# Performance work log

Measured on AMD Instinct MI355X. Metric: run time of the kernel, lower is better.

The kernel has to match this reference:

```python
import jax, jax.numpy as jnp
import numpy as np
from jax.scipy.special import logsumexp

NUM_JOINT_TYPES = 17
SINKHORN_ITERS = 30
SINKHORN_TAU = 0.05
BIG_COST = 1.0e6


def _scot_forward(embeddings, W1, b1, prototype_pool, joint_types, k):
    n = embeddings.shape[0]
    # node encoder: Linear + SELU
    h = jax.nn.selu(embeddings @ W1 + b1)  # [N, H]
    prototypes = prototype_pool[:k]        # [K, H] (k <= k_max)
    # squared euclidean distance (torch.cdist(p=2).pow(2))
    d2 = (jnp.sum(h * h, axis=1)[:, None]
          + jnp.sum(prototypes * prototypes, axis=1)[None, :]
          - 2.0 * (h @ prototypes.T))
    d2 = jnp.maximum(d2, 0.0)              # [N, K]
    # expand each person slot to 17 joint-type slots
    cost = jnp.repeat(d2, NUM_JOINT_TYPES, axis=1)          # [N, K*17]
    slot_types = jnp.tile(jnp.arange(NUM_JOINT_TYPES), k)   # [K*17]
    type_mask = joint_types[:, None] == slot_types[None, :]  # [N, K*17]
    cost = jnp.where(type_mask, cost, BIG_COST)

    n_slots = k * NUM_JOINT_TYPES
    log_K = -cost / SINKHORN_TAU
    log_K_ext = jnp.concatenate([log_K, jnp.zeros((n, 1), log_K.dtype)], axis=1)  # [N, K*17+1]
    # target marginal: 1 per slot, slack column absorbs leftover mass
    tm = jnp.ones(n_slots + 1, log_K.dtype).at[-1].set(float(max(n - n_slots, 1)))
    log_tm = jnp.log(tm)

    def step(carry, _):
        log_u, log_v = carry
        log_u = -logsumexp(log_K_ext + log_v[None, :], axis=1)   # row normalization
        log_v = log_tm - logsumexp(log_K_ext + log_u[:, None], axis=0)  # col normalization
        return (log_u, log_v), None

    init = (jnp.zeros(n, log_K.dtype), jnp.zeros(n_slots + 1, log_K.dtype))
    (log_u, log_v), _ = jax.lax.scan(step, init, None, length=SINKHORN_ITERS)

    T = jnp.exp(log_K_ext + log_u[:, None] + log_v[None, :])[:, :n_slots]  # [N, K*17]
    logits = jnp.log(T.reshape(n, k, NUM_JOINT_TYPES).sum(axis=2) + 1e-8)  # [N, K]
    return logits, T


def setup_inputs() -> dict:
    key = jax.random.key(0)
    k_emb, k_w, k_proto, k_jt = jax.random.split(key, 4)
    N, D, H, KMAX = 6144, 256, 256, 512
    emb = jax.random.normal(k_emb, (N, D), dtype=jnp.float32)
    emb = emb / jnp.linalg.norm(emb, axis=1, keepdims=True)  # L2-normalised per docstring
    W1 = jax.random.normal(k_w, (D, H), dtype=jnp.float32) * (1.0 / np.sqrt(D))
    b1 = jnp.zeros((H,), jnp.float32)
    prototype_pool = jax.random.normal(k_proto, (KMAX, H), dtype=jnp.float32) * 0.5
    joint_types = jax.random.randint(k_jt, (N,), 0, NUM_JOINT_TYPES)
    return {"embeddings": emb, "W1": W1, "b1": b1,
            "prototype_pool": prototype_pool, "joint_types": joint_types, "k": 300}


def reference(embeddings, W1, b1, prototype_pool, joint_types, k):
    return _scot_forward(embeddings, W1, b1, prototype_pool, joint_types, k)
```

## Files before the change

kernel.cpp:

```cpp
#include <hip/hip_runtime.h>
#include <math.h>

#define NT 17
#define NB 17
#define KCAP 300
#define KP 320
#define NITER 30
#define MSCALE2 28.853900817779268f

typedef unsigned long long u64;
typedef float vfloat4 __attribute__((ext_vector_type(4)));

#define EX2(x) __builtin_amdgcn_exp2f(x)
#define LG2(x) __builtin_amdgcn_logf(x)
#if __has_builtin(__builtin_amdgcn_rcpf)
#define RCP(x) __builtin_amdgcn_rcpf(x)
#else
#define RCP(x) (1.0f / (x))
#endif

__device__ inline unsigned bf16rne(float x) {
  unsigned u = __float_as_uint(x);
  return (u + 0x7FFFu + ((u >> 16) & 1u)) >> 16;
}
__device__ inline unsigned bfp(float lo, float hi) {
  return bf16rne(lo) | (bf16rne(hi) << 16);
}
#define BFLO(p) __uint_as_float((p) << 16)
#define BFHI(p) __uint_as_float((p) & 0xFFFF0000u)


__device__ inline float selu_f(float x) {
  const float scale = 1.0507009873554804934193349852946f;
  const float alpha = 1.6732632423543772848170429916717f;
  return x > 0.f ? scale * x : scale * alpha * (EX2(x * 1.4426950408889634f) - 1.f);
}

__global__ __launch_bounds__(1024) void k_bucket(const int* __restrict__ jt, int n,
    int* __restrict__ meta, int* __restrict__ perm, int* __restrict__ tys) {
  __shared__ int hist[NT];
  __shared__ int off[NT];
  __shared__ int cnt[NT];
  int tid = threadIdx.x;
  if (tid < NT) { hist[tid] = 0; cnt[tid] = 0; }
  __syncthreads();
  for (int i = tid; i < n; i += 1024) atomicAdd(&hist[jt[i]], 1);
  __syncthreads();
  if (tid == 0) {
    int o = 0;
    for (int t = 0; t < NT; t++) {
      off[t] = o; meta[32 + t] = o; meta[t] = hist[t]; o += hist[t];
    }
  }
  __syncthreads();
  for (int i = tid; i < n; i += 1024) {
    int t = jt[i];
    int pos = off[t] + atomicAdd(&cnt[t], 1);
    perm[pos] = i;
    tys[pos] = t;
  }
}

__global__ __launch_bounds__(256) void k_hgemm(const float* __restrict__ A,
    const float* __restrict__ B, const float* __restrict__ bias,
    float* __restrict__ C, int n, int D, int H) {
  __shared__ __align__(16) float As[16][68];
  __shared__ __align__(16) float Bs[16][68];
  int tid = threadIdx.x;
  int i0 = blockIdx.x * 64, j0 = blockIdx.y * 64;
  int tx = tid & 15, ty = tid >> 4;
  int aI = tid & 63, aK = (tid >> 6) << 2;
  int bJ = (tid & 15) << 2, bK = tid >> 4;
  float acc[4][4] = {};
  for (int k0 = 0; k0 < D; k0 += 16) {
    float4 av = *(const float4*)(A + (size_t)(i0 + aI) * D + k0 + aK);
    float4 bv = *(const float4*)(B + (size_t)(k0 + bK) * H + j0 + bJ);
    __syncthreads();
    As[aK + 0][aI] = av.x; As[aK + 1][aI] = av.y; As[aK + 2][aI] = av.z; As[aK + 3][aI] = av.w;
    *(float4*)(&Bs[bK][bJ]) = bv;
    __syncthreads();
#pragma unroll
    for (int kk = 0; kk < 16; kk++) {
      float4 a4 = *(float4*)(&As[kk][ty << 2]);
      float4 b4 = *(float4*)(&Bs[kk][tx << 2]);
      float aa[4] = {a4.x, a4.y, a4.z, a4.w};
      float bb[4] = {b4.x, b4.y, b4.z, b4.w};
#pragma unroll
      for (int p = 0; p < 4; p++)
#pragma unroll
        for (int q = 0; q < 4; q++)
          acc[p][q] = fmaf(aa[p], bb[q], acc[p][q]);
    }
  }
#pragma unroll
  for (int p = 0; p < 4; p++) {
    int i = i0 + (ty << 2) + p;
    float o[4];
#pragma unroll
    for (int q = 0; q < 4; q++) {
      int j = j0 + (tx << 2) + q;
      o[q] = selu_f(acc[p][q] + bias[j]);
    }
    *(float4*)(C + (size_t)i * H + j0 + (tx << 2)) = make_float4(o[0], o[1], o[2], o[3]);
  }
}

__global__ __launch_bounds__(256) void k_msort(const float* __restrict__ h,
    const float* __restrict__ P, const int* __restrict__ perm,
    float* __restrict__ Ms, int n, int H, int k) {
  __shared__ __align__(16) float As[16][68];
  __shared__ __align__(16) float Bs[16][68];
  __shared__ float hp[4][64];
  __shared__ float pp[4][64];
  __shared__ int gIdx[64];
  int tid = threadIdx.x;
  int i0 = blockIdx.x * 64, j0 = blockIdx.y * 64;
  if (tid < 64) gIdx[tid] = perm[i0 + tid];
  __syncthreads();
  int tx = tid & 15, ty = tid >> 4;
  int aI = tid & 63, aK = (tid >> 6) << 2;
  int gA = gIdx[aI];
  bool bok = (j0 + aI) < k;
  const float* bRow = P + (size_t)(j0 + (bok ? aI : 0)) * H;
  float acc[4][4] = {};
  float ha = 0.f, pa = 0.f;
  for (int k0 = 0; k0 < H; k0 += 16) {
    float4 av = *(const float4*)(h + (size_t)gA * H + k0 + aK);
    float4 bv = *(const float4*)(bRow + k0 + aK);
    ha += av.x * av.x + av.y * av.y + av.z * av.z + av.w * av.w;
    pa += bv.x * bv.x + bv.y * bv.y + bv.z * bv.z + bv.w * bv.w;
    __syncthreads();
    As[aK + 0][aI] = av.x; As[aK + 1][aI] = av.y; As[aK + 2][aI] = av.z; As[aK + 3][aI] = av.w;
    Bs[aK + 0][aI] = bv.x; Bs[aK + 1][aI] = bv.y; Bs[aK + 2][aI] = bv.z; Bs[aK + 3][aI] = bv.w;
    __syncthreads();
#pragma unroll
    for (int kk = 0; kk < 16; kk++) {
      float4 a4 = *(float4*)(&As[kk][ty << 2]);
      float4 b4 = *(float4*)(&Bs[kk][tx << 2]);
      float aa[4] = {a4.x, a4.y, a4.z, a4.w};
      float bb[4] = {b4.x, b4.y, b4.z, b4.w};
#pragma unroll
      for (int p = 0; p < 4; p++)
#pragma unroll
        for (int q = 0; q < 4; q++)
          acc[p][q] = fmaf(aa[p], bb[q], acc[p][q]);
    }
  }
  int grp = tid >> 6;
  hp[grp][aI] = ha;
  pp[grp][aI] = pa;
  __syncthreads();
#pragma unroll
  for (int p = 0; p < 4; p++) {
    int rr = (ty << 2) + p;
    int r = i0 + rr;
    float hq = hp[0][rr] + hp[1][rr] + hp[2][rr] + hp[3][rr];
#pragma unroll
    for (int q = 0; q < 4; q++) {
      int jl = (tx << 2) + q;
      int j = j0 + jl;
      if (j < k) {
        float pq = pp[0][jl] + pp[1][jl] + pp[2][jl] + pp[3][jl];
        float d2 = hq + pq - 2.f * acc[p][q];
        d2 = fmaxf(d2, 0.f);
        Ms[(size_t)r * k + j] = -d2 * MSCALE2;
      }
    }
  }
}

__global__ __launch_bounds__(1024) void k_sink(const float* __restrict__ Ms,
    unsigned short* __restrict__ Ms2,
    const int* __restrict__ meta,
    float* __restrict__ suD, unsigned* __restrict__ suE,
    float* __restrict__ uF, float* __restrict__ vF,
    int k, float tm_last) {
  __shared__ __align__(16) float V[KP];
  __shared__ __align__(16) float WP2[16][KP];
  __shared__ float uarr[1024];
  __shared__ float SU[16];
  __shared__ float w_sh;
  __shared__ int lvl_ep;
  int tid = threadIdx.x, lane = tid & 63, wv = tid >> 6;
  int t = blockIdx.x;
  int myR = meta[t];
  int s0 = meta[32 + t];
  int nt = (myR + 3) >> 2;
  bool l2v = (lane + 64) < (k >> 2);
  int g = lane >> 4, cg = lane & 15;
  bool r2 = (cg < 8);
  const char* ms2 = (const char*)Ms2;

  if (tid == 0) { w_sh = 1.f; lvl_ep = 0; }

  {
    float4 cm0 = make_float4(-3e38f, -3e38f, -3e38f, -3e38f);
    float4 cm1 = cm0;
    for (int tile = wv; tile < nt; tile += 16) {
      int r0 = tile * 4;
#pragma unroll
      for (int rr = 0; rr < 4; rr++) {
        int rc = (r0 + rr < myR) ? (r0 + rr) : r0;
        const float4* rp = (const float4*)(Ms + (size_t)(s0 + rc) * k);
        float4 a0 = rp[lane];
        cm0.x = fmaxf(cm0.x, a0.x); cm0.y = fmaxf(cm0.y, a0.y);
        cm0.z = fmaxf(cm0.z, a0.z); cm0.w = fmaxf(cm0.w, a0.w);
        if (l2v) {
          float4 a1 = rp[lane + 64];
          cm1.x = fmaxf(cm1.x, a1.x); cm1.y = fmaxf(cm1.y, a1.y);
          cm1.z = fmaxf(cm1.z, a1.z); cm1.w = fmaxf(cm1.w, a1.w);
        }
      }
    }
    *(float4*)&WP2[wv][4 * lane] = cm0;
    if (l2v) *(float4*)&WP2[wv][4 * (lane + 64)] = cm1;
    __syncthreads();
    if (tid < k) {
      float cmax = WP2[0][tid];
#pragma unroll
      for (int q = 1; q < 16; q++) cmax = fmaxf(cmax, WP2[q][tid]);
      V[tid] = cmax;
    }
    __syncthreads();
    float4 cx0 = *(const float4*)&V[4 * lane];
    float4 cx1 = l2v ? *(const float4*)&V[4 * (lane + 64)] : cx0;
    for (int tile = wv; tile < nt; tile += 16) {
      int r0 = tile * 4;
#pragma unroll
      for (int rr = 0; rr < 4; rr++) {
        int r = r0 + rr;
        if (r < myR) {
          const float4* rp = (const float4*)(Ms + (size_t)(s0 + r) * k);
          char* orow = (char*)Ms2 + (size_t)(s0 + r) * (KP * 2);
          float4 a0 = rp[lane];
          uint2 o;
          o.x = bfp(EX2(a0.x - cx0.x), EX2(a0.y - cx0.y));
          o.y = bfp(EX2(a0.z - cx0.z), EX2(a0.w - cx0.w));
          *(uint2*)(orow + 8 * lane) = o;
          if (l2v) {
            float4 a1 = rp[lane + 64];
            uint2 o1;
            o1.x = bfp(EX2(a1.x - cx1.x), EX2(a1.y - cx1.y));
            o1.y = bfp(EX2(a1.z - cx1.z), EX2(a1.w - cx1.w));
            *(uint2*)(orow + 512 + 8 * lane) = o1;
          } else if (lane < 16) {
            *(uint2*)(orow + 512 + 8 * lane) = make_uint2(0u, 0u);
          }
        }
      }
    }
  }
  __syncthreads();
  if (tid < KP) V[tid] = 0.f;
  __syncthreads();

  for (int m = 0; m < NITER; m++) {
    int epoch = m + 1;
    int slot = m & 3;
    if (wv == 15) {
      if (m > 0) {
        int pslot = (m - 1) & 3;
        unsigned want = (unsigned)m;
        bool need = lane < NB;
        for (;;) {
          bool ok = !need ||
              (__hip_atomic_load(&suE[(pslot * NB + lane) * 16],
                                 __ATOMIC_RELAXED, __HIP_MEMORY_SCOPE_AGENT) >= want);
          if (__all(ok)) break;
          __builtin_amdgcn_s_sleep(1);
        }
        float s = need
            ? __hip_atomic_load(&suD[(pslot * NB + lane) * 16],
                                __ATOMIC_RELAXED, __HIP_MEMORY_SCOPE_AGENT)
            : 0.f;
#pragma unroll
        for (int o = 32; o; o >>= 1) s += __shfl_xor(s, o);
        if (lane == 0) w_sh = tm_last / s;
      }
      if (lane == 0)
        __hip_atomic_store(&lvl_ep, epoch, __ATOMIC_RELEASE, __HIP_MEMORY_SCOPE_WORKGROUP);
    }
    float w = 0.f;
    bool haveW = (wv == 15);
    float su = 0.f;
    float vv[3][8];
#pragma unroll
    for (int q3 = 0; q3 < 3; q3++) {
      if (q3 < 2 || r2) {
        float4 x0 = *(const float4*)&V[q3 * 128 + cg * 8];
        float4 x1 = *(const float4*)&V[q3 * 128 + cg * 8 + 4];
        vv[q3][0] = x0.x; vv[q3][1] = x0.y; vv[q3][2] = x0.z; vv[q3][3] = x0.w;
        vv[q3][4] = x1.x; vv[q3][5] = x1.y; vv[q3][6] = x1.z; vv[q3][7] = x1.w;
      } else {
#pragma unroll
        for (int e = 0; e < 8; e++) vv[q3][e] = 0.f;
      }
    }
    float acc[3][8];
#pragma unroll
    for (int q3 = 0; q3 < 3; q3++)
#pragma unroll
      for (int e = 0; e < 8; e++) acc[q3][e] = 0.f;
    uint4 Ta[3], Tb[3];

    auto loadTile = [&](int tile, uint4 (&T)[3]) {
      int r = tile * 4 + g;
      int rc = (r < myR) ? r : 0;
      const char* p = ms2 + (size_t)(s0 + rc) * (KP * 2) + (cg << 4);
      T[0] = *(const uint4*)(p);
      T[1] = *(const uint4*)(p + 256);
      T[2] = make_uint4(0u, 0u, 0u, 0u);
      if (r2) T[2] = *(const uint4*)(p + 512);
    };
    auto computeTile = [&](int tile, uint4 (&T)[3]) {
      int r = tile * 4 + g;
      float rs = 0.f;
#pragma unroll
      for (int q3 = 0; q3 < 3; q3++) {
        rs = fmaf(BFLO(T[q3].x), vv[q3][0], rs);
        rs = fmaf(BFHI(T[q3].x), vv[q3][1], rs);
        rs = fmaf(BFLO(T[q3].y), vv[q3][2], rs);
        rs = fmaf(BFHI(T[q3].y), vv[q3][3], rs);
        rs = fmaf(BFLO(T[q3].z), vv[q3][4], rs);
        rs = fmaf(BFHI(T[q3].z), vv[q3][5], rs);
        rs = fmaf(BFLO(T[q3].w), vv[q3][6], rs);
        rs = fmaf(BFHI(T[q3].w), vv[q3][7], rs);
      }
      rs += __shfl_xor(rs, 1); rs += __shfl_xor(rs, 2);
      rs += __shfl_xor(rs, 4); rs += __shfl_xor(rs, 8);
      if (!haveW) {
        while (__hip_atomic_load(&lvl_ep, __ATOMIC_ACQUIRE, __HIP_MEMORY_SCOPE_WORKGROUP) < epoch)
          __builtin_amdgcn_s_sleep(1);
        w = w_sh;
        haveW = true;
      }
      bool valid = (r < myR);
      float u = RCP(rs + w);
      float uu = valid ? u : 0.f;
      if (cg == 0) {
        su += uu;
        if (valid) uarr[r] = u;
      }
#pragma unroll
      for (int q3 = 0; q3 < 3; q3++) {
        acc[q3][0] = fmaf(BFLO(T[q3].x), uu, acc[q3][0]);
        acc[q3][1] = fmaf(BFHI(T[q3].x), uu, acc[q3][1]);
        acc[q3][2] = fmaf(BFLO(T[q3].y), uu, acc[q3][2]);
        acc[q3][3] = fmaf(BFHI(T[q3].y), uu, acc[q3][3]);
        acc[q3][4] = fmaf(BFLO(T[q3].z), uu, acc[q3][4]);
        acc[q3][5] = fmaf(BFHI(T[q3].z), uu, acc[q3][5]);
        acc[q3][6] = fmaf(BFLO(T[q3].w), uu, acc[q3][6]);
        acc[q3][7] = fmaf(BFHI(T[q3].w), uu, acc[q3][7]);
      }
    };

    int tile = (wv < 15) ? wv : nt;
    if (tile < nt) loadTile(tile, Ta);
    while (tile < nt) {
      int n1 = tile + 15;
      if (n1 < nt) loadTile(n1, Tb);
      computeTile(tile, Ta);
      if (n1 < nt) {
        int n2 = n1 + 15;
        if (n2 < nt) loadTile(n2, Ta);
        computeTile(n1, Tb);
      }
      tile += 30;
    }
    if (!haveW) {
      while (__hip_atomic_load(&lvl_ep, __ATOMIC_ACQUIRE, __HIP_MEMORY_SCOPE_WORKGROUP) < epoch)
        __builtin_amdgcn_s_sleep(1);
      haveW = true;
    }

    if (wv < 15) {
#pragma unroll
      for (int q3 = 0; q3 < 3; q3++)
#pragma unroll
        for (int e = 0; e < 8; e++) {
          float a = acc[q3][e];
          a += __shfl_xor(a, 16);
          a += __shfl_xor(a, 32);
          acc[q3][e] = a;
        }
      if (lane < 16) {
#pragma unroll
        for (int q3 = 0; q3 < 3; q3++) {
          if (q3 < 2 || lane < 8) {
            *(float4*)&WP2[wv][q3 * 128 + lane * 8] =
                make_float4(acc[q3][0], acc[q3][1], acc[q3][2], acc[q3][3]);
            *(float4*)&WP2[wv][q3 * 128 + lane * 8 + 4] =
                make_float4(acc[q3][4], acc[q3][5], acc[q3][6], acc[q3][7]);
          }
        }
      }
      float sr = su;
      sr += __shfl_xor(sr, 16);
      sr += __shfl_xor(sr, 32);
      if (lane == 0) SU[wv] = sr;
    }
    __syncthreads();
    if (tid < KP) {
      float s = WP2[0][tid];
#pragma unroll
      for (int q = 1; q < 15; q++) s += WP2[q][tid];
      V[tid] = (tid < k) ? RCP(s) : 0.f;
    }
    if (wv == 15) {
      float sp = (lane < 15) ? SU[lane] : 0.f;
#pragma unroll
      for (int o = 32; o; o >>= 1) sp += __shfl_xor(sp, o);
      if (lane == 0)
        __hip_atomic_store(&suD[(slot * NB + t) * 16], sp,
                           __ATOMIC_RELAXED, __HIP_MEMORY_SCOPE_AGENT);
      __builtin_amdgcn_s_waitcnt(0);
      if (lane == 0)
        __hip_atomic_store(&suE[(slot * NB + t) * 16], (unsigned)epoch,
                           __ATOMIC_RELAXED, __HIP_MEMORY_SCOPE_AGENT);
    }
    __syncthreads();
  }
  for (int r = tid; r < myR; r += 1024) uF[s0 + r] = uarr[r];
  for (int j = tid; j < k; j += 1024) vF[(size_t)t * k + j] = V[j];
}

__global__ __launch_bounds__(256) void k_epi(const unsigned short* __restrict__ Ms2,
    const float* __restrict__ uF, const float* __restrict__ vF,
    const int* __restrict__ perm, const int* __restrict__ tys,
    float* __restrict__ out, int n, int k) {
  __shared__ float vals[KCAP];
  int r = blockIdx.x;
  int i = perm[r], t = tys[r];
  float u = uF[r];
  const unsigned short* Krow = Ms2 + (size_t)r * KP;
  const float* Vrow = vF + (size_t)t * k;
  for (int j = threadIdx.x; j < k; j += 256)
    vals[j] = __uint_as_float((unsigned)Krow[j] << 16) * u * Vrow[j];
  __syncthreads();
  float* lg = out + (size_t)i * k;
  for (int j = threadIdx.x; j < k; j += 256)
    __builtin_nontemporal_store(LG2(vals[j] + 1e-8f) * 0.6931471805599453f, &lg[j]);
  int ns = k * NT;
  float* Trow = out + (size_t)n * k + (size_t)i * ns;
  if ((ns & 3) == 0) {
    int n4 = ns >> 2;
    int o0 = threadIdx.x << 2;
    int rmod = o0 % NT;
    for (int g4 = threadIdx.x; g4 < n4; g4 += 256, o0 += 1024) {
      int sstar = t - rmod; if (sstar < 0) sstar += NT;
      int j = (unsigned)(o0 + sstar) / (unsigned)NT;
      float vv = vals[j < k ? j : 0];
      vfloat4 v;
      v.x = (sstar == 0) ? vv : 0.f;
      v.y = (sstar == 1) ? vv : 0.f;
      v.z = (sstar == 2) ? vv : 0.f;
      v.w = (sstar == 3) ? vv : 0.f;
      __builtin_nontemporal_store(v, (vfloat4*)(Trow + o0));
      rmod += 4; if (rmod >= NT) rmod -= NT;
    }
  } else {
    for (int o = threadIdx.x; o < ns; o += 256) {
      int j = o / NT;
      int tt = o - j * NT;
      Trow[o] = (tt == t) ? vals[j] : 0.f;
    }
  }
}

extern "C" void kernel_launch(void* const* d_in, const int* in_sizes, int n_in,
                              void* d_out, int out_size, void* d_ws, size_t ws_size,
                              hipStream_t stream) {
  const float* emb = (const float*)d_in[0];
  const float* W1  = (const float*)d_in[1];
  const float* b1  = (const float*)d_in[2];
  const float* P   = (const float*)d_in[3];
  const int*   jt  = (const int*)d_in[4];
  (void)n_in; (void)ws_size;

  const int n = in_sizes[4];
  const int H = in_sizes[2];
  const int D = in_sizes[1] / H;
  const int k = out_size / (n * (NT + 1));
  const int nslots = k * NT;
  const float tm_last = (float)((n - nslots) > 1 ? (n - nslots) : 1);

  char* w = (char*)d_ws;
  size_t off = 0;
  auto take = [&](size_t bytes) -> char* {
    char* p = w + off;
    off = (off + bytes + 255) & ~(size_t)255;
    return p;
  };
  int*      meta = (int*)take(4096);
  int*      perm = (int*)take((size_t)n * 4);
  int*      tys  = (int*)take((size_t)n * 4);
  float*    h    = (float*)take((size_t)n * H * 4);
  float*    Ms   = (float*)take((size_t)n * k * 4);
  unsigned short* Ms2 = (unsigned short*)take((size_t)n * KP * 2 + 1024);
  float*    suD  = (float*)take((size_t)4 * NB * 64);
  unsigned* suE  = (unsigned*)take((size_t)4 * NB * 64);
  float*    uF   = (float*)take((size_t)n * 4);
  float*    vF   = (float*)take((size_t)NT * k * 4);

  (void)hipMemsetAsync(suE, 0, (size_t)4 * NB * 64, stream);
  k_bucket<<<1, 1024, 0, stream>>>(jt, n, meta, perm, tys);
  k_hgemm<<<dim3(n / 64, H / 64), dim3(256), 0, stream>>>(emb, W1, b1, h, n, D, H);
  k_msort<<<dim3(n / 64, (k + 63) / 64), dim3(256), 0, stream>>>(h, P, perm, Ms, n, H, k);
  k_sink<<<NB, 1024, 0, stream>>>(Ms, Ms2, meta, suD, suE, uF, vF, k, tm_last);
  k_epi<<<n, 256, 0, stream>>>(Ms2, uF, vF, perm, tys, (float*)d_out, n, k);
}
```

Before: 466.6 us.

## Split each joint-type Sinkhorn block into paired halves with LDS-cached kernel rows

The Sinkhorn kernel now launches two workgroups per joint type instead of one. Each handles half the rows and exchanges column maxima and per-iteration column partial sums with its partner through global atomics and flag spin-waits. Each block also caches up to 208 bf16 kernel rows in LDS so most per-iteration row reads avoid global memory, and u values are written directly on the last iteration. This doubles the CUs in use and reduces global traffic, at the cost of an extra cross-block handshake every iteration and heavy LDS use.

```diff
diff --git a/kernel.cpp b/kernel.cpp
--- a/kernel.cpp
+++ b/kernel.cpp
@@ -2,9 +2,11 @@
 #include <math.h>
 
 #define NT 17
-#define NB 17
+#define NBLK 34
 #define KCAP 300
 #define KP 320
+#define LCAP 208
+#define CH 2
 #define NITER 30
 #define MSCALE2 28.853900817779268f
 
@@ -170,33 +172,41 @@
 }
 
 __global__ __launch_bounds__(1024) void k_sink(const float* __restrict__ Ms,
-    unsigned short* __restrict__ Ms2,
-    const int* __restrict__ meta,
+    unsigned short* __restrict__ Ms2, const int* __restrict__ meta,
+    float* __restrict__ cmD, unsigned* __restrict__ cmE,
+    float* __restrict__ pcD, unsigned* __restrict__ pcE,
     float* __restrict__ suD, unsigned* __restrict__ suE,
     float* __restrict__ uF, float* __restrict__ vF,
     int k, float tm_last) {
+  __shared__ __align__(16) unsigned short Klds[LCAP * KP];
+  __shared__ __align__(16) float WP2[16][KP];
   __shared__ __align__(16) float V[KP];
-  __shared__ __align__(16) float WP2[16][KP];
-  __shared__ float uarr[1024];
+  __shared__ __align__(16) float Sown[KP];
   __shared__ float SU[16];
   __shared__ float w_sh;
   __shared__ int lvl_ep;
+  __shared__ int pairflag;
   int tid = threadIdx.x, lane = tid & 63, wv = tid >> 6;
-  int t = blockIdx.x;
-  int myR = meta[t];
-  int s0 = meta[32 + t];
-  int nt = (myR + 3) >> 2;
+  int c = blockIdx.x;
+  int t = c >> 1, hb = c & 1, prt = c ^ 1;
+  int cRt = meta[t];
+  int s0t = meta[32 + t];
+  int h0 = (cRt + 1) >> 1;
+  int rb = hb ? h0 : 0;
+  int re = hb ? cRt : h0;
+  int myR = re - rb;
+  int s0 = s0t + rb;
+  int ntH = (myR + 3) >> 2;
   bool l2v = (lane + 64) < (k >> 2);
   int g = lane >> 4, cg = lane & 15;
-  bool r2 = (cg < 8);
-  const char* ms2 = (const char*)Ms2;
-
-  if (tid == 0) { w_sh = 1.f; lvl_ep = 0; }
+  bool r2a = (cg < 8);
+
+  if (tid == 0) { w_sh = 1.f; lvl_ep = 0; pairflag = 0; }
 
   {
     float4 cm0 = make_float4(-3e38f, -3e38f, -3e38f, -3e38f);
     float4 cm1 = cm0;
-    for (int tile = wv; tile < nt; tile += 16) {
+    for (int tile = wv; tile < ntH; tile += 16) {
       int r0 = tile * 4;
 #pragma unroll
       for (int rr = 0; rr < 4; rr++) {
@@ -219,12 +229,28 @@
       float cmax = WP2[0][tid];
 #pragma unroll
       for (int q = 1; q < 16; q++) cmax = fmaxf(cmax, WP2[q][tid]);
-      V[tid] = cmax;
+      Sown[tid] = cmax;
+      __hip_atomic_store(&cmD[c * KP + tid], cmax,
+                         __ATOMIC_RELAXED, __HIP_MEMORY_SCOPE_AGENT);
+    }
+    __syncthreads();
+    if (tid == 0) {
+      __hip_atomic_store(&cmE[c * 16], 1u, __ATOMIC_RELAXED, __HIP_MEMORY_SCOPE_AGENT);
+      while (__hip_atomic_load(&cmE[prt * 16], __ATOMIC_RELAXED, __HIP_MEMORY_SCOPE_AGENT) < 1u)
+        __builtin_amdgcn_s_sleep(1);
+      __hip_atomic_store(&pairflag, 1, __ATOMIC_RELEASE, __HIP_MEMORY_SCOPE_WORKGROUP);
+    }
+    if (tid < k) {
+      while (__hip_atomic_load(&pairflag, __ATOMIC_ACQUIRE, __HIP_MEMORY_SCOPE_WORKGROUP) < 1)
+        __builtin_amdgcn_s_sleep(1);
+      float o = __hip_atomic_load(&cmD[prt * KP + tid],
+                                  __ATOMIC_RELAXED, __HIP_MEMORY_SCOPE_AGENT);
+      V[tid] = fmaxf(Sown[tid], o);
     }
     __syncthreads();
     float4 cx0 = *(const float4*)&V[4 * lane];
     float4 cx1 = l2v ? *(const float4*)&V[4 * (lane + 64)] : cx0;
-    for (int tile = wv; tile < nt; tile += 16) {
+    for (int tile = wv; tile < ntH; tile += 16) {
       int r0 = tile * 4;
 #pragma unroll
       for (int rr = 0; rr < 4; rr++) {
@@ -232,19 +258,24 @@
         if (r < myR) {
           const float4* rp = (const float4*)(Ms + (size_t)(s0 + r) * k);
           char* orow = (char*)Ms2 + (size_t)(s0 + r) * (KP * 2);
+          char* lrow = (char*)Klds + (size_t)r * (KP * 2);
+          bool inL = (r < LCAP);
           float4 a0 = rp[lane];
           uint2 o;
           o.x = bfp(EX2(a0.x - cx0.x), EX2(a0.y - cx0.y));
           o.y = bfp(EX2(a0.z - cx0.z), EX2(a0.w - cx0.w));
           *(uint2*)(orow + 8 * lane) = o;
+          if (inL) *(uint2*)(lrow + 8 * lane) = o;
           if (l2v) {
             float4 a1 = rp[lane + 64];
             uint2 o1;
             o1.x = bfp(EX2(a1.x - cx1.x), EX2(a1.y - cx1.y));
             o1.y = bfp(EX2(a1.z - cx1.z), EX2(a1.w - cx1.w));
             *(uint2*)(orow + 512 + 8 * lane) = o1;
+            if (inL) *(uint2*)(lrow + 512 + 8 * lane) = o1;
           } else if (lane < 16) {
             *(uint2*)(orow + 512 + 8 * lane) = make_uint2(0u, 0u);
+            if (inL) *(uint2*)(lrow + 512 + 8 * lane) = make_uint2(0u, 0u);
           }
         }
       }
@@ -261,16 +292,16 @@
       if (m > 0) {
         int pslot = (m - 1) & 3;
         unsigned want = (unsigned)m;
-        bool need = lane < NB;
+        bool need = lane < NBLK;
         for (;;) {
           bool ok = !need ||
-              (__hip_atomic_load(&suE[(pslot * NB + lane) * 16],
+              (__hip_atomic_load(&suE[(pslot * NBLK + lane) * 16],
                                  __ATOMIC_RELAXED, __HIP_MEMORY_SCOPE_AGENT) >= want);
           if (__all(ok)) break;
           __builtin_amdgcn_s_sleep(1);
         }
         float s = need
-            ? __hip_atomic_load(&suD[(pslot * NB + lane) * 16],
+            ? __hip_atomic_load(&suD[(pslot * NBLK + lane) * 16],
                                 __ATOMIC_RELAXED, __HIP_MEMORY_SCOPE_AGENT)
             : 0.f;
 #pragma unroll
@@ -286,7 +317,7 @@
     float vv[3][8];
 #pragma unroll
     for (int q3 = 0; q3 < 3; q3++) {
-      if (q3 < 2 || r2) {
+      if (q3 < 2 || r2a) {
         float4 x0 = *(const float4*)&V[q3 * 128 + cg * 8];
         float4 x1 = *(const float4*)&V[q3 * 128 + cg * 8 + 4];
         vv[q3][0] = x0.x; vv[q3][1] = x0.y; vv[q3][2] = x0.z; vv[q3][3] = x0.w;
@@ -301,71 +332,80 @@
     for (int q3 = 0; q3 < 3; q3++)
 #pragma unroll
       for (int e = 0; e < 8; e++) acc[q3][e] = 0.f;
-    uint4 Ta[3], Tb[3];
-
-    auto loadTile = [&](int tile, uint4 (&T)[3]) {
-      int r = tile * 4 + g;
-      int rc = (r < myR) ? r : 0;
-      const char* p = ms2 + (size_t)(s0 + rc) * (KP * 2) + (cg << 4);
-      T[0] = *(const uint4*)(p);
-      T[1] = *(const uint4*)(p + 256);
-      T[2] = make_uint4(0u, 0u, 0u, 0u);
-      if (r2) T[2] = *(const uint4*)(p + 512);
-    };
-    auto computeTile = [&](int tile, uint4 (&T)[3]) {
-      int r = tile * 4 + g;
-      float rs = 0.f;
-#pragma unroll
-      for (int q3 = 0; q3 < 3; q3++) {
-        rs = fmaf(BFLO(T[q3].x), vv[q3][0], rs);
-        rs = fmaf(BFHI(T[q3].x), vv[q3][1], rs);
-        rs = fmaf(BFLO(T[q3].y), vv[q3][2], rs);
-        rs = fmaf(BFHI(T[q3].y), vv[q3][3], rs);
-        rs = fmaf(BFLO(T[q3].z), vv[q3][4], rs);
-        rs = fmaf(BFHI(T[q3].z), vv[q3][5], rs);
-        rs = fmaf(BFLO(T[q3].w), vv[q3][6], rs);
-        rs = fmaf(BFHI(T[q3].w), vv[q3][7], rs);
-      }
-      rs += __shfl_xor(rs, 1); rs += __shfl_xor(rs, 2);
-      rs += __shfl_xor(rs, 4); rs += __shfl_xor(rs, 8);
+
+    int t0 = (wv < 15) ? wv : ntH;
+    for (; t0 < ntH; t0 += 15 * CH) {
+      uint4 T[CH][3];
+      float rs[CH];
+#pragma unroll
+      for (int ccc = 0; ccc < CH; ccc++) {
+        int tile = t0 + 15 * ccc;
+        rs[ccc] = 0.f;
+        if (tile < ntH) {
+          int r = tile * 4 + g;
+          int rc = (r < myR) ? r : (myR - 1);
+          uint4 z4 = make_uint4(0u, 0u, 0u, 0u);
+          if (rc < LCAP) {
+            const uint4* lp = (const uint4*)((const char*)Klds +
+                (size_t)rc * (KP * 2) + (cg << 4));
+            T[ccc][0] = lp[0];
+            T[ccc][1] = lp[16];
+            if (r2a) T[ccc][2] = lp[32]; else T[ccc][2] = z4;
+          } else {
+            const uint4* gp = (const uint4*)((const char*)Ms2 +
+                (size_t)(s0 + rc) * (KP * 2) + (cg << 4));
+            T[ccc][0] = gp[0];
+            T[ccc][1] = gp[16];
+            if (r2a) T[ccc][2] = gp[32]; else T[ccc][2] = z4;
+          }
+          float r1 = 0.f;
+#pragma unroll
+          for (int q3 = 0; q3 < 3; q3++) {
+            r1 = fmaf(BFLO(T[ccc][q3].x), vv[q3][0], r1);
+            r1 = fmaf(BFHI(T[ccc][q3].x), vv[q3][1], r1);
+            r1 = fmaf(BFLO(T[ccc][q3].y), vv[q3][2], r1);
+            r1 = fmaf(BFHI(T[ccc][q3].y), vv[q3][3], r1);
+            r1 = fmaf(BFLO(T[ccc][q3].z), vv[q3][4], r1);
+            r1 = fmaf(BFHI(T[ccc][q3].z), vv[q3][5], r1);
+            r1 = fmaf(BFLO(T[ccc][q3].w), vv[q3][6], r1);
+            r1 = fmaf(BFHI(T[ccc][q3].w), vv[q3][7], r1);
+          }
+          r1 += __shfl_xor(r1, 1); r1 += __shfl_xor(r1, 2);
+          r1 += __shfl_xor(r1, 4); r1 += __shfl_xor(r1, 8);
+          rs[ccc] = r1;
+        }
+      }
       if (!haveW) {
         while (__hip_atomic_load(&lvl_ep, __ATOMIC_ACQUIRE, __HIP_MEMORY_SCOPE_WORKGROUP) < epoch)
           __builtin_amdgcn_s_sleep(1);
         w = w_sh;
         haveW = true;
       }
-      bool valid = (r < myR);
-      float u = RCP(rs + w);
-      float uu = valid ? u : 0.f;
-      if (cg == 0) {
-        su += uu;
-        if (valid) uarr[r] = u;
-      }
-#pragma unroll
-      for (int q3 = 0; q3 < 3; q3++) {
-        acc[q3][0] = fmaf(BFLO(T[q3].x), uu, acc[q3][0]);
-        acc[q3][1] = fmaf(BFHI(T[q3].x), uu, acc[q3][1]);
-        acc[q3][2] = fmaf(BFLO(T[q3].y), uu, acc[q3][2]);
-        acc[q3][3] = fmaf(BFHI(T[q3].y), uu, acc[q3][3]);
-        acc[q3][4] = fmaf(BFLO(T[q3].z), uu, acc[q3][4]);
-        acc[q3][5] = fmaf(BFHI(T[q3].z), uu, acc[q3][5]);
-        acc[q3][6] = fmaf(BFLO(T[q3].w), uu, acc[q3][6]);
-        acc[q3][7] = fmaf(BFHI(T[q3].w), uu, acc[q3][7]);
-      }
-    };
-
-    int tile = (wv < 15) ? wv : nt;
-    if (tile < nt) loadTile(tile, Ta);
-    while (tile < nt) {
-      int n1 = tile + 15;
-      if (n1 < nt) loadTile(n1, Tb);
-      computeTile(tile, Ta);
-      if (n1 < nt) {
-        int n2 = n1 + 15;
-        if (n2 < nt) loadTile(n2, Ta);
-        computeTile(n1, Tb);
-      }
-      tile += 30;
+#pragma unroll
+      for (int ccc = 0; ccc < CH; ccc++) {
+        int tile = t0 + 15 * ccc;
+        if (tile < ntH) {
+          int r = tile * 4 + g;
+          bool valid = (r < myR);
+          float u = RCP(rs[ccc] + w);
+          float uu = valid ? u : 0.f;
+          if (cg == 0) {
+            su += uu;
+            if (valid && m == NITER - 1) uF[s0 + r] = u;
+          }
+#pragma unroll
+          for (int q3 = 0; q3 < 3; q3++) {
+            acc[q3][0] = fmaf(BFLO(T[ccc][q3].x), uu, acc[q3][0]);
+            acc[q3][1] = fmaf(BFHI(T[ccc][q3].x), uu, acc[q3][1]);
+            acc[q3][2] = fmaf(BFLO(T[ccc][q3].y), uu, acc[q3][2]);
+            acc[q3][3] = fmaf(BFHI(T[ccc][q3].y), uu, acc[q3][3]);
+            acc[q3][4] = fmaf(BFLO(T[ccc][q3].z), uu, acc[q3][4]);
+            acc[q3][5] = fmaf(BFHI(T[ccc][q3].z), uu, acc[q3][5]);
+            acc[q3][6] = fmaf(BFLO(T[ccc][q3].w), uu, acc[q3][6]);
+            acc[q3][7] = fmaf(BFHI(T[ccc][q3].w), uu, acc[q3][7]);
+          }
+        }
+      }
     }
     if (!haveW) {
       while (__hip_atomic_load(&lvl_ep, __ATOMIC_ACQUIRE, __HIP_MEMORY_SCOPE_WORKGROUP) < epoch)
@@ -400,28 +440,46 @@
       if (lane == 0) SU[wv] = sr;
     }
     __syncthreads();
-    if (tid < KP) {
+    if (tid < k) {
       float s = WP2[0][tid];
 #pragma unroll
       for (int q = 1; q < 15; q++) s += WP2[q][tid];
-      V[tid] = (tid < k) ? RCP(s) : 0.f;
+      Sown[tid] = s;
+      __hip_atomic_store(&pcD[(slot * NBLK + c) * KP + tid], s,
+                         __ATOMIC_RELAXED, __HIP_MEMORY_SCOPE_AGENT);
     }
     if (wv == 15) {
       float sp = (lane < 15) ? SU[lane] : 0.f;
 #pragma unroll
       for (int o = 32; o; o >>= 1) sp += __shfl_xor(sp, o);
       if (lane == 0)
-        __hip_atomic_store(&suD[(slot * NB + t) * 16], sp,
+        __hip_atomic_store(&suD[(slot * NBLK + c) * 16], sp,
                            __ATOMIC_RELAXED, __HIP_MEMORY_SCOPE_AGENT);
       __builtin_amdgcn_s_waitcnt(0);
       if (lane == 0)
-        __hip_atomic_store(&suE[(slot * NB + t) * 16], (unsigned)epoch,
+        __hip_atomic_store(&suE[(slot * NBLK + c) * 16], (unsigned)epoch,
                            __ATOMIC_RELAXED, __HIP_MEMORY_SCOPE_AGENT);
     }
     __syncthreads();
-  }
-  for (int r = tid; r < myR; r += 1024) uF[s0 + r] = uarr[r];
-  for (int j = tid; j < k; j += 1024) vF[(size_t)t * k + j] = V[j];
+    if (tid == 0) {
+      __hip_atomic_store(&pcE[(slot * NBLK + c) * 16], (unsigned)epoch,
+                         __ATOMIC_RELAXED, __HIP_MEMORY_SCOPE_AGENT);
+      while (__hip_atomic_load(&pcE[(slot * NBLK + prt) * 16],
+                               __ATOMIC_RELAXED, __HIP_MEMORY_SCOPE_AGENT) < (unsigned)epoch)
+        __builtin_amdgcn_s_sleep(1);
+      __hip_atomic_store(&pairflag, m + 2, __ATOMIC_RELEASE, __HIP_MEMORY_SCOPE_WORKGROUP);
+    }
+    if (tid < k) {
+      while (__hip_atomic_load(&pairflag, __ATOMIC_ACQUIRE, __HIP_MEMORY_SCOPE_WORKGROUP) < m + 2)
+        __builtin_amdgcn_s_sleep(1);
+      float sp = __hip_atomic_load(&pcD[(slot * NBLK + prt) * KP + tid],
+                                   __ATOMIC_RELAXED, __HIP_MEMORY_SCOPE_AGENT);
+      V[tid] = RCP(Sown[tid] + sp);
+    }
+    __syncthreads();
+  }
+  if (hb == 0)
+    for (int j = tid; j < k; j += 1024) vF[(size_t)t * k + j] = V[j];
 }
 
 __global__ __launch_bounds__(256) void k_epi(const unsigned short* __restrict__ Ms2,
@@ -497,15 +555,22 @@
   float*    h    = (float*)take((size_t)n * H * 4);
   float*    Ms   = (float*)take((size_t)n * k * 4);
   unsigned short* Ms2 = (unsigned short*)take((size_t)n * KP * 2 + 1024);
-  float*    suD  = (float*)take((size_t)4 * NB * 64);
-  unsigned* suE  = (unsigned*)take((size_t)4 * NB * 64);
+  float*    cmD  = (float*)take((size_t)NBLK * KP * 4);
+  unsigned* cmE  = (unsigned*)take((size_t)NBLK * 64);
+  float*    pcD  = (float*)take((size_t)4 * NBLK * KP * 4);
+  unsigned* pcE  = (unsigned*)take((size_t)4 * NBLK * 64);
+  float*    suD  = (float*)take((size_t)4 * NBLK * 64);
+  unsigned* suE  = (unsigned*)take((size_t)4 * NBLK * 64);
   float*    uF   = (float*)take((size_t)n * 4);
   float*    vF   = (float*)take((size_t)NT * k * 4);
 
-  (void)hipMemsetAsync(suE, 0, (size_t)4 * NB * 64, stream);
+  (void)hipMemsetAsync(cmE, 0, (size_t)NBLK * 64, stream);
+  (void)hipMemsetAsync(pcE, 0, (size_t)4 * NBLK * 64, stream);
+  (void)hipMemsetAsync(suE, 0, (size_t)4 * NBLK * 64, stream);
   k_bucket<<<1, 1024, 0, stream>>>(jt, n, meta, perm, tys);
   k_hgemm<<<dim3(n / 64, H / 64), dim3(256), 0, stream>>>(emb, W1, b1, h, n, D, H);
   k_msort<<<dim3(n / 64, (k + 63) / 64), dim3(256), 0, stream>>>(h, P, perm, Ms, n, H, k);
-  k_sink<<<NB, 1024, 0, stream>>>(Ms, Ms2, meta, suD, suE, uF, vF, k, tm_last);
+  k_sink<<<NBLK, 1024, 0, stream>>>(Ms, Ms2, meta, cmD, cmE, pcD, pcE,
+                                    suD, suE, uF, vF, k, tm_last);
   k_epi<<<n, 256, 0, stream>>>(Ms2, uF, vF, perm, tys, (float*)d_out, n, k);
 }
```

Measured after the change: 424.1 us. 9.1% less time.
